# Kernel tuning notes

Hardware: AMD Instinct MI355X
Metric: run time of the kernel (lower is better)

The kernel has to match this reference:

```python
import jax, jax.numpy as jnp
import numpy as np

B, C_EDGE, C_FUSED, C_SEM = 4, 64, 128, 128
H = W = 64
MASK_SIZE = 11
EPS = 1e-6


def _window_mask(h, w, mask_size):
    # M_dw: 0 inside the clipped (mask_size x mask_size) window around each query pixel, -10000 outside.
    half = mask_size // 2
    idx = jnp.arange(h * w)
    qx, qy = idx // w, idx % w
    inside = (jnp.abs(qx[:, None] - qx[None, :]) <= half) & (jnp.abs(qy[:, None] - qy[None, :]) <= half)
    return jnp.where(inside, 0.0, -10000.0).astype(jnp.float32)


def _conv1x1(x, w, b):
    # x: [b, cin, h, w], w: [cout, cin]
    return jnp.einsum('bchw,oc->bohw', x, w) + b[None, :, None, None]


def _proj1d(x, w, b):
    # x: [b, cin, n], w: [cout, cin]
    return jnp.einsum('bcn,oc->bon', x, w) + b[None, :, None]


def _bilinear(x, h, w):
    # matches F.interpolate(mode='bilinear', align_corners=False)
    b, c = x.shape[0], x.shape[1]
    return jax.image.resize(x, (b, c, h, w), method='linear', antialias=False)


def setup_inputs() -> dict:
    key = jax.random.key(0)
    ks = jax.random.split(key, 13)
    s = 0.05
    return {
        'edge_features': jax.random.normal(ks[0], (B, C_EDGE, 32, 32), jnp.float32),
        'semantic_features': jax.random.normal(ks[1], (B, C_SEM, H, W), jnp.float32),
        'fused_features': jax.random.normal(ks[2], (B, C_FUSED, 32, 32), jnp.float32),
        'w_align': jax.random.normal(ks[3], (C_SEM, C_EDGE), jnp.float32) * s,
        'b_align': jax.random.normal(ks[4], (C_SEM,), jnp.float32) * s,
        'w_fused_align': jax.random.normal(ks[5], (C_SEM, C_FUSED), jnp.float32) * s,
        'b_fused_align': jax.random.normal(ks[6], (C_SEM,), jnp.float32) * s,
        'w_q': jax.random.normal(ks[7], (2 * C_SEM, 2 * C_SEM), jnp.float32) * s,
        'b_q': jax.random.normal(ks[8], (2 * C_SEM,), jnp.float32) * s,
        'w_k': jax.random.normal(ks[9], (2 * C_SEM, 2 * C_SEM), jnp.float32) * s,
        'b_k': jax.random.normal(ks[10], (2 * C_SEM,), jnp.float32) * s,
        'w_fusion': jax.random.normal(ks[11], (C_SEM, 2 * C_SEM), jnp.float32) * s,
        'b_fusion': jax.random.normal(ks[12], (C_SEM,), jnp.float32) * s,
    }


def reference(edge_features, semantic_features, fused_features,
              w_align, b_align, w_fused_align, b_fused_align,
              w_q, b_q, w_k, b_k, w_fusion, b_fusion):
    b, c, h, w = semantic_features.shape
    n = h * w

    edge = _conv1x1(_bilinear(edge_features, h, w), w_align, b_align)            # [b,c,h,w]
    fused = _conv1x1(_bilinear(fused_features, h, w), w_fused_align, b_fused_align)

    l2_edge = jnp.sqrt(jnp.sum(edge * edge, axis=1, keepdims=True))              # [b,1,h,w]
    l2_sem = jnp.sqrt(jnp.sum(semantic_features * semantic_features, axis=1, keepdims=True))
    similarity = jnp.sum((edge / (l2_edge + EPS)) * (semantic_features / (l2_sem + EPS)),
                         axis=1, keepdims=True)
    similarity = (similarity + 1.0) * 0.5

    density_flat = l2_edge.reshape(b, n)
    density = (jax.nn.softmax(density_flat, axis=1) * n).reshape(b, 1, h, w)

    edge_t = (edge * similarity).reshape(b, c, n)
    sem_t = (semantic_features * density).reshape(b, c, n)
    fused_t = fused.reshape(b, c, n)
    sem_raw = semantic_features.reshape(b, c, n)

    edge_cat = jnp.concatenate([edge_t, edge_t], axis=1)    # [b,2c,n]
    sem_cat = jnp.concatenate([sem_t, fused_t], axis=1)
    sem_val = jnp.concatenate([sem_raw, fused_t], axis=1)

    q = _proj1d(edge_cat, w_q, b_q)                          # [b,2c,n]
    k = _proj1d(sem_cat, w_k, b_k)

    scale = 1.0 / jnp.sqrt(jnp.float32(2 * c))
    attn = jnp.einsum('bcn,bcm->bnm', q, k) * scale          # [b,n,n]
    attn = attn + _window_mask(h, w, MASK_SIZE)
    attn = jax.nn.softmax(attn, axis=-1)

    out = jnp.einsum('bnm,bcm->bnc', attn, sem_val)          # [b,n,2c]
    out = out.reshape(b, h, w, 2 * c).transpose(0, 3, 1, 2)  # [b,2c,h,w]
    return _conv1x1(out, w_fusion, b_fusion)
```

## Files before the change

kernel.cpp:

```cpp
#include <hip/hip_runtime.h>
#include <hip/hip_bf16.h>

#define NB 4
#define C 128
#define N 4096
#define EPS 1e-6f
#define PW 80
#define PIMG 5120

typedef float f32x4 __attribute__((ext_vector_type(4)));
typedef short bf16x8 __attribute__((ext_vector_type(8)));
typedef unsigned short ushort_t;
typedef unsigned int uint_t;

__device__ __forceinline__ ushort_t f2bf(float f) {
  __hip_bfloat16 h = __float2bfloat16(f);
  return *reinterpret_cast<ushort_t*>(&h);
}

struct alignas(8) us4 { ushort_t a, b, c, d; };

__device__ __forceinline__ void conv_body(const float* __restrict__ x,
                                          const float* __restrict__ w,
                                          const float* __restrict__ bias,
                                          float* __restrict__ out,
                                          int n, int o0, int b, int CIN) {
  const float* xb = x + (size_t)(b * CIN) * 1024 + n;
  float a0 = 0.f, a1 = 0.f, a2 = 0.f, a3 = 0.f;
  for (int c = 0; c < CIN; ++c) {
    float xv = xb[(size_t)c * 1024];
    a0 += w[(o0 + 0) * CIN + c] * xv;
    a1 += w[(o0 + 1) * CIN + c] * xv;
    a2 += w[(o0 + 2) * CIN + c] * xv;
    a3 += w[(o0 + 3) * CIN + c] * xv;
  }
  size_t ob = ((size_t)b * 128 + o0) * 1024 + n;
  out[ob]        = a0 + bias[o0];
  out[ob + 1024] = a1 + bias[o0 + 1];
  out[ob + 2048] = a2 + bias[o0 + 2];
  out[ob + 3072] = a3 + bias[o0 + 3];
}

__global__ void prep_misc(const float* __restrict__ edge_f, const float* __restrict__ w_align,
                          const float* __restrict__ b_align,
                          const float* __restrict__ fused_f, const float* __restrict__ w_fal,
                          const float* __restrict__ b_fal,
                          const float* __restrict__ wq, const float* __restrict__ wk,
                          const float* __restrict__ wf,
                          ushort_t* __restrict__ wqf, ushort_t* __restrict__ wkf,
                          ushort_t* __restrict__ wff,
                          float* __restrict__ edge32, float* __restrict__ fused32,
                          float* __restrict__ dsum) {
  int bx = blockIdx.x, t = threadIdx.x;
  if (bx < 64) {
    if (bx == 0 && t < NB) dsum[t] = 0.f;
    int c = bx * 256 + t;
    int lane = c & 63;
    int mrow = lane & 15, quad = lane >> 4;
    if (c < 4096) {
      int grp = c >> 6;
      int tile = grp >> 2, kslot = grp & 3;
      int o = tile * 16 + mrow, k0 = kslot * 32 + quad * 8;
      const float* s = wq + o * 256 + k0;
      ushort_t* d = wqf + (size_t)c * 8;
#pragma unroll
      for (int j = 0; j < 8; ++j) d[j] = f2bf(s[j] + s[128 + j]);
    } else if (c < 12288) {
      int c2 = c - 4096;
      int grp = c2 >> 6;
      int tile = grp >> 3, kslot = grp & 7;
      int o = tile * 16 + mrow, k0 = kslot * 32 + quad * 8;
      const float* s = wk + o * 256 + k0;
      ushort_t* d = wkf + (size_t)c2 * 8;
#pragma unroll
      for (int j = 0; j < 8; ++j) d[j] = f2bf(s[j]);
    } else {
      int c2 = c - 12288;
      int grp = c2 >> 6;
      int tile = grp >> 3, kslot = grp & 7;
      int o = tile * 16 + mrow, k0 = kslot * 32 + quad * 8;
      const float* s = wf + o * 256 + k0;
      ushort_t* d = wff + (size_t)c2 * 8;
#pragma unroll
      for (int j = 0; j < 8; ++j) d[j] = f2bf(s[j]);
    }
  } else if (bx < 576) {
    int j = bx - 64;
    conv_body(edge_f, w_align, b_align, edge32, (j & 3) * 256 + t, ((j >> 2) & 31) * 4, j >> 7, 64);
  } else {
    int j = bx - 576;
    conv_body(fused_f, w_fal, b_fal, fused32, (j & 3) * 256 + t, ((j >> 2) & 31) * 4, j >> 7, 128);
  }
}

__global__ __launch_bounds__(256) void prep_acts(const float* __restrict__ edge32,
                                                 const float* __restrict__ fused32,
                                                 const float* __restrict__ sem,
                                                 ushort_t* __restrict__ xt_edge,
                                                 ushort_t* __restrict__ xt_sem,
                                                 ushort_t* __restrict__ xt_fused,
                                                 float* __restrict__ simb,
                                                 float* __restrict__ l2e,
                                                 float* __restrict__ dsum) {
  int b = blockIdx.y, bx = blockIdx.x;
  int y = bx >> 1, xh = (bx & 1) * 32;
  int t = threadIdx.x;
  int nl = t & 31, cg = t >> 5;
  int x = xh + nl;
  int yy0 = (y & 1) ? (y >> 1) : (y >> 1) - 1;
  float fy = (y & 1) ? 0.25f : 0.75f;
  int y0c = max(yy0, 0), y1c = min(yy0 + 1, 31);
  int xx0 = (x & 1) ? (x >> 1) : (x >> 1) - 1;
  float fx = (x & 1) ? 0.25f : 0.75f;
  int x0c = max(xx0, 0), x1c = min(xx0 + 1, 31);

  __shared__ uint_t se[32][65], ssm[32][65], sf[32][65];
  __shared__ float red[4][3][32];

  float ee = 0.f, ssum = 0.f, es = 0.f;
#pragma unroll 2
  for (int p = 0; p < 8; ++p) {
    float evs[2], fvs[2], svs[2];
#pragma unroll
    for (int u = 0; u < 2; ++u) {
      int c = cg * 16 + p * 2 + u;
      const float* ip = edge32 + ((size_t)(b * 128 + c)) * 1024;
      float e00 = ip[y0c * 32 + x0c], e01 = ip[y0c * 32 + x1c];
      float e10 = ip[y1c * 32 + x0c], e11 = ip[y1c * 32 + x1c];
      float ev = (1.f - fy) * ((1.f - fx) * e00 + fx * e01) + fy * ((1.f - fx) * e10 + fx * e11);
      const float* fp = fused32 + ((size_t)(b * 128 + c)) * 1024;
      float f00 = fp[y0c * 32 + x0c], f01 = fp[y0c * 32 + x1c];
      float f10 = fp[y1c * 32 + x0c], f11 = fp[y1c * 32 + x1c];
      float fv = (1.f - fy) * ((1.f - fx) * f00 + fx * f01) + fy * ((1.f - fx) * f10 + fx * f11);
      float sv = sem[((size_t)(b * 128 + c)) * 4096 + y * 64 + x];
      ee += ev * ev; ssum += sv * sv; es += ev * sv;
      evs[u] = ev; fvs[u] = fv; svs[u] = sv;
    }
    int col = cg * 8 + p;
    se[nl][col]  = (uint_t)f2bf(evs[0]) | ((uint_t)f2bf(evs[1]) << 16);
    sf[nl][col]  = (uint_t)f2bf(fvs[0]) | ((uint_t)f2bf(fvs[1]) << 16);
    ssm[nl][col] = (uint_t)f2bf(svs[0]) | ((uint_t)f2bf(svs[1]) << 16);
  }
  ee += __shfl_xor(ee, 32, 64); ssum += __shfl_xor(ssum, 32, 64); es += __shfl_xor(es, 32, 64);
  int w = t >> 6, lane = t & 63;
  if (lane < 32) { red[w][0][lane] = ee; red[w][1][lane] = ssum; red[w][2][lane] = es; }
  __syncthreads();
  int base_n = b * 4096 + y * 64 + xh;
#pragma unroll
  for (int rep = 0; rep < 8; ++rep) {
    int d = rep * 256 + t;
    int r = d >> 6, cp = d & 63;
    ((uint_t*)xt_edge)[(size_t)(base_n + r) * 64 + cp] = se[r][cp];
    ((uint_t*)xt_sem)[(size_t)(base_n + r) * 64 + cp] = ssm[r][cp];
    ((uint_t*)xt_fused)[(size_t)(base_n + r) * 64 + cp] = sf[r][cp];
  }
  if (t < 32) {
    float E = 0.f, S = 0.f, X = 0.f;
#pragma unroll
    for (int w2 = 0; w2 < 4; ++w2) { E += red[w2][0][t]; S += red[w2][1][t]; X += red[w2][2][t]; }
    float le = sqrtf(E), ls = sqrtf(S);
    simb[base_n + t] = (X / ((le + EPS) * (ls + EPS)) + 1.f) * 0.5f;
    l2e[base_n + t] = le;
    float pe = expf(le - 16.f);
#pragma unroll
    for (int m2 = 16; m2; m2 >>= 1) pe += __shfl_xor(pe, m2, 64);
    if (t == 0) atomicAdd(&dsum[b], pe);
  }
}

__global__ __launch_bounds__(256) void gemm_kv(const ushort_t* __restrict__ xt_sem,
                                               const ushort_t* __restrict__ xt_fused,
                                               const ushort_t* __restrict__ wkf,
                                               const ushort_t* __restrict__ wff,
                                               const float* __restrict__ b_k,
                                               const float* __restrict__ l2e,
                                               const float* __restrict__ dsum,
                                               ushort_t* __restrict__ ktb,
                                               ushort_t* __restrict__ v2b) {
  int bx = blockIdx.x, bI = blockIdx.y;
  int t = threadIdx.x, w = t >> 6, lane = t & 63;
  int mrow = lane & 15, quad = lane >> 4;
  __shared__ __align__(16) ushort_t stg[16896];

  if (bx < 64) {
    int y = bx, n0 = y * 64, o0 = w * 64;
    float dscale = 4096.f / dsum[bI];
    for (int nt = 0; nt < 4; ++nt) {
      int n0t = n0 + nt * 16;
      const ushort_t* bS = xt_sem + ((size_t)bI * N + n0t + mrow) * 128 + quad * 8;
      const ushort_t* bF = xt_fused + ((size_t)bI * N + n0t + mrow) * 128 + quad * 8;
      f32x4 accL[4], accR[4];
#pragma unroll
      for (int i = 0; i < 4; ++i) { accL[i] = (f32x4){0.f,0.f,0.f,0.f}; accR[i] = (f32x4){0.f,0.f,0.f,0.f}; }
#pragma unroll
      for (int kk = 0; kk < 4; ++kk) {
        bf16x8 bfr = *(const bf16x8*)(bS + kk * 32);
#pragma unroll
        for (int i = 0; i < 4; ++i) {
          bf16x8 afr = *(const bf16x8*)(wkf + (size_t)((((w * 4 + i) * 8) + kk) * 64 + lane) * 8);
          accL[i] = __builtin_amdgcn_mfma_f32_16x16x32_bf16(afr, bfr, accL[i], 0, 0, 0);
        }
      }
#pragma unroll
      for (int kk = 0; kk < 4; ++kk) {
        bf16x8 bfr = *(const bf16x8*)(bF + kk * 32);
#pragma unroll
        for (int i = 0; i < 4; ++i) {
          bf16x8 afr = *(const bf16x8*)(wkf + (size_t)((((w * 4 + i) * 8) + 4 + kk) * 64 + lane) * 8);
          accR[i] = __builtin_amdgcn_mfma_f32_16x16x32_bf16(afr, bfr, accR[i], 0, 0, 0);
        }
      }
      int n = n0t + mrow;
      float dv = expf(l2e[bI * N + n] - 16.f) * dscale;
#pragma unroll
      for (int i = 0; i < 4; ++i) {
        int o = o0 + i * 16 + quad * 4;
        float4 bk = *(const float4*)(b_k + o);
        us4 pk = { f2bf(accL[i][0] * dv + accR[i][0] + bk.x),
                   f2bf(accL[i][1] * dv + accR[i][1] + bk.y),
                   f2bf(accL[i][2] * dv + accR[i][2] + bk.z),
                   f2bf(accL[i][3] * dv + accR[i][3] + bk.w) };
        *(us4*)&stg[(nt * 16 + mrow) * 264 + o] = pk;
      }
    }
    __syncthreads();
    int np0 = y * PW + 8;
#pragma unroll
    for (int r = 0; r < 8; ++r) {
      int cidx = r * 256 + t;
      int row = cidx >> 5, cc = cidx & 31;
      *(bf16x8*)(ktb + ((size_t)bI * PIMG + np0 + row) * 256 + cc * 8) =
          *(const bf16x8*)&stg[row * 264 + cc * 8];
    }
  } else {
    int y = bx - 64, n0 = y * 64, o0 = w * 32;
    for (int nt = 0; nt < 4; ++nt) {
      int n0t = n0 + nt * 16;
      const ushort_t* bS = xt_sem + ((size_t)bI * N + n0t + mrow) * 128 + quad * 8;
      const ushort_t* bF = xt_fused + ((size_t)bI * N + n0t + mrow) * 128 + quad * 8;
      f32x4 accL[2], accR[2];
#pragma unroll
      for (int i = 0; i < 2; ++i) { accL[i] = (f32x4){0.f,0.f,0.f,0.f}; accR[i] = (f32x4){0.f,0.f,0.f,0.f}; }
#pragma unroll
      for (int kk = 0; kk < 4; ++kk) {
        bf16x8 bfr = *(const bf16x8*)(bS + kk * 32);
#pragma unroll
        for (int i = 0; i < 2; ++i) {
          bf16x8 afr = *(const bf16x8*)(wff + (size_t)((((w * 2 + i) * 8) + kk) * 64 + lane) * 8);
          accL[i] = __builtin_amdgcn_mfma_f32_16x16x32_bf16(afr, bfr, accL[i], 0, 0, 0);
        }
      }
#pragma unroll
      for (int kk = 0; kk < 4; ++kk) {
        bf16x8 bfr = *(const bf16x8*)(bF + kk * 32);
#pragma unroll
        for (int i = 0; i < 2; ++i) {
          bf16x8 afr = *(const bf16x8*)(wff + (size_t)((((w * 2 + i) * 8) + 4 + kk) * 64 + lane) * 8);
          accR[i] = __builtin_amdgcn_mfma_f32_16x16x32_bf16(afr, bfr, accR[i], 0, 0, 0);
        }
      }
#pragma unroll
      for (int i = 0; i < 2; ++i) {
#pragma unroll
        for (int r = 0; r < 4; ++r) {
          int ch = o0 + i * 16 + quad * 4 + r;
          stg[ch * 72 + nt * 16 + mrow] = f2bf(accL[i][r] + accR[i][r]);
        }
      }
    }
    __syncthreads();
    int np0 = y * PW + 8;
#pragma unroll
    for (int r = 0; r < 4; ++r) {
      int cidx = r * 256 + t;
      int ch = cidx >> 3, seg = cidx & 7;
      *(bf16x8*)(v2b + ((size_t)bI * 128 + ch) * PIMG + np0 + seg * 8) =
          *(const bf16x8*)&stg[ch * 72 + seg * 8];
    }
  }
}

__global__ __launch_bounds__(256) void attn_kernel(const ushort_t* __restrict__ xt_edge,
                                                   const ushort_t* __restrict__ wqf,
                                                   const float* __restrict__ b_q,
                                                   const float* __restrict__ simb,
                                                   const ushort_t* __restrict__ ktb,
                                                   const ushort_t* __restrict__ v2b,
                                                   const float* __restrict__ b_fusion,
                                                   float* __restrict__ out) {
  int L = blockIdx.x;
  int xcd = L & 7, j = L >> 3;
  int b = xcd >> 1;
  int ty0 = (((xcd & 1) << 3) + (j >> 4)) * 4;
  int tx0 = (j & 15) * 4;
  int y0 = max(ty0 - 5, 0), y1 = min(ty0 + 8, 63);
  int nh = y1 - y0 + 1;
  int x0a = tx0 - 8 - ((tx0 & 4) ? 4 : 0);
  int cb = x0a + 8;
  int ntq = (nh * 3 + 1) >> 1;
  int npv = (nh * 3 + 3) >> 2;

  __shared__ ushort_t pst[16][352];
  __shared__ __align__(16) ushort_t qs[4096];
  __shared__ float redm[4][16], reds[4][16];

  int t = threadIdx.x, w = t >> 6, lane = t & 63;
  int l15 = lane & 15, quad = lane >> 4;

  if (ntq * 16 < npv * 32) pst[t & 15][ntq * 16 + (t >> 4)] = 0;

  int nq_l = (ty0 + (l15 >> 2)) * 64 + tx0 + (l15 & 3);

  {
    const ushort_t* bp = xt_edge + ((size_t)b * N + nq_l) * 128 + quad * 8;
    f32x4 qacc[4];
#pragma unroll
    for (int i = 0; i < 4; ++i) qacc[i] = (f32x4){0.f, 0.f, 0.f, 0.f};
#pragma unroll
    for (int kk = 0; kk < 4; ++kk) {
      bf16x8 bfr = *(const bf16x8*)(bp + kk * 32);
#pragma unroll
      for (int i = 0; i < 4; ++i) {
        bf16x8 afr = *(const bf16x8*)(wqf + (size_t)((((w * 4 + i) * 4) + kk) * 64 + lane) * 8);
        qacc[i] = __builtin_amdgcn_mfma_f32_16x16x32_bf16(afr, bfr, qacc[i], 0, 0, 0);
      }
    }
    float sv = simb[b * N + nq_l];
#pragma unroll
    for (int i = 0; i < 4; ++i) {
      int o = w * 64 + i * 16 + quad * 4;
      float4 bq = *(const float4*)(b_q + o);
      us4 pk = { f2bf(sv * qacc[i][0] + bq.x), f2bf(sv * qacc[i][1] + bq.y),
                 f2bf(sv * qacc[i][2] + bq.z), f2bf(sv * qacc[i][3] + bq.w) };
      int kk2 = o >> 5, q2 = (o >> 3) & 3;
      int lane2 = l15 + 16 * q2;
      *(us4*)&qs[((kk2 * 64 + lane2) * 8) + (o & 7)] = pk;
    }
  }
  __syncthreads();

  bf16x8 qfr[8];
#pragma unroll
  for (int ks = 0; ks < 8; ++ks) qfr[ks] = *(const bf16x8*)&qs[(ks * 64 + lane) * 8];

  int qy = ty0 + (l15 >> 2), qx = tx0 + (l15 & 3);

  const ushort_t* kb = ktb + (size_t)b * PIMG * 256;
  f32x4 sc[6];
#pragma unroll
  for (int i = 0; i < 6; ++i) {
    int tq = w + i * 4;
    if (tq >= ntq) break;
    int key = tq * 16 + l15;
    int ry = (key * 2731) >> 16;
    int rx = key - ry * 24;
    int yy = min(y0 + ry, 63);
    const ushort_t* krow = kb + (size_t)(yy * PW + cb + rx) * 256 + quad * 8;
    f32x4 acc = (f32x4){0.f, 0.f, 0.f, 0.f};
#pragma unroll
    for (int ks = 0; ks < 8; ++ks) {
      bf16x8 afr = *(const bf16x8*)(krow + ks * 32);
      acc = __builtin_amdgcn_mfma_f32_16x16x32_bf16(afr, qfr[ks], acc, 0, 0, 0);
    }
    sc[i] = acc;
  }
  float mymax = -1e30f;
#pragma unroll
  for (int i = 0; i < 6; ++i) {
    int tq = w + i * 4;
    if (tq >= ntq) break;
#pragma unroll
    for (int r = 0; r < 4; ++r) {
      int key = tq * 16 + quad * 4 + r;
      int ry = (key * 2731) >> 16;
      int rx = key - ry * 24;
      int x = x0a + rx;
      int dy = y0 + ry - qy, dx = x - qx;
      float s = -1e30f;
      if (ry < nh && dy >= -5 && dy <= 5 && dx >= -5 && dx <= 5 && x >= 0 && x <= 63)
        s = sc[i][r] * 0.0625f;
      sc[i][r] = s;
      mymax = fmaxf(mymax, s);
    }
  }
  mymax = fmaxf(mymax, __shfl_xor(mymax, 16, 64));
  mymax = fmaxf(mymax, __shfl_xor(mymax, 32, 64));
  if (quad == 0) redm[w][l15] = mymax;
  __syncthreads();
  float gmax = fmaxf(fmaxf(redm[0][l15], redm[1][l15]), fmaxf(redm[2][l15], redm[3][l15]));
  float mysum = 0.f;
#pragma unroll
  for (int i = 0; i < 6; ++i) {
    int tq = w + i * 4;
    if (tq >= ntq) break;
#pragma unroll
    for (int r = 0; r < 4; ++r) {
      float e = expf(sc[i][r] - gmax);
      sc[i][r] = e;
      mysum += e;
    }
  }
  mysum += __shfl_xor(mysum, 16, 64);
  mysum += __shfl_xor(mysum, 32, 64);
  if (quad == 0) reds[w][l15] = mysum;
#pragma unroll
  for (int i = 0; i < 6; ++i) {
    int tq = w + i * 4;
    if (tq >= ntq) break;
    uint_t p01 = (uint_t)f2bf(sc[i][0]) | ((uint_t)f2bf(sc[i][1]) << 16);
    uint_t p23 = (uint_t)f2bf(sc[i][2]) | ((uint_t)f2bf(sc[i][3]) << 16);
    *(uint_t*)(&pst[l15][tq * 16 + quad * 4]) = p01;
    *(uint_t*)(&pst[l15][tq * 16 + quad * 4 + 2]) = p23;
  }
  __syncthreads();

  float rinv = 1.f / (reds[0][l15] + reds[1][l15] + reds[2][l15] + reds[3][l15]);

  const ushort_t* vb = v2b + (size_t)b * 128 * PIMG;
#pragma unroll
  for (int half = 0; half < 2; ++half) {
    int ch0 = half * 64 + w * 16;
    const ushort_t* vrow = vb + (size_t)(ch0 + l15) * PIMG;
    f32x4 acc = (f32x4){0.f, 0.f, 0.f, 0.f};
    for (int ks = 0; ks < npv; ++ks) {
      int kst = ks * 32 + quad * 8;
      int ry = (kst * 2731) >> 16;
      int rxs = kst - ry * 24;
      int yy = min(y0 + ry, 63);
      bf16x8 av = *(const bf16x8*)(vrow + yy * PW + cb + rxs);
      bf16x8 bp2 = *(const bf16x8*)(&pst[l15][kst]);
      acc = __builtin_amdgcn_mfma_f32_16x16x32_bf16(av, bp2, acc, 0, 0, 0);
    }
    int chg = ch0 + quad * 4;
#pragma unroll
    for (int r = 0; r < 4; ++r)
      out[((size_t)b * 128 + chg + r) * N + nq_l] = acc[r] * rinv + b_fusion[chg + r];
  }
}

extern "C" void kernel_launch(void* const* d_in, const int* in_sizes, int n_in,
                              void* d_out, int out_size, void* d_ws, size_t ws_size,
                              hipStream_t stream) {
  (void)in_sizes; (void)n_in; (void)out_size; (void)ws_size;
  const float* edge_f  = (const float*)d_in[0];
  const float* sem     = (const float*)d_in[1];
  const float* fused_f = (const float*)d_in[2];
  const float* w_align = (const float*)d_in[3];
  const float* b_align = (const float*)d_in[4];
  const float* w_fal   = (const float*)d_in[5];
  const float* b_fal   = (const float*)d_in[6];
  const float* w_q     = (const float*)d_in[7];
  const float* b_q     = (const float*)d_in[8];
  const float* w_k     = (const float*)d_in[9];
  const float* b_k     = (const float*)d_in[10];
  const float* w_fus   = (const float*)d_in[11];
  const float* b_fus   = (const float*)d_in[12];
  float* out = (float*)d_out;

  float* ws = (float*)d_ws;
  float* edge32   = ws;
  float* fused32  = ws + 524288;
  float* simb     = ws + 1048576;
  float* l2e      = ws + 1064960;
  float* dsum     = ws + 1081344;
  ushort_t* xt_edge  = (ushort_t*)(ws + 1097728);
  ushort_t* xt_sem   = (ushort_t*)(ws + 2146304);
  ushort_t* xt_fused = (ushort_t*)(ws + 3194880);
  ushort_t* wqf      = (ushort_t*)(ws + 4243456);
  ushort_t* wkf      = (ushort_t*)(ws + 4259840);
  ushort_t* wff      = (ushort_t*)(ws + 4292608);
  ushort_t* ktb      = (ushort_t*)(ws + 4308992);
  ushort_t* v2b      = (ushort_t*)(ws + 6930432);

  prep_misc<<<1088, 256, 0, stream>>>(edge_f, w_align, b_align, fused_f, w_fal, b_fal,
                                      w_q, w_k, w_fus, wqf, wkf, wff, edge32, fused32, dsum);
  prep_acts<<<dim3(128, NB), 256, 0, stream>>>(edge32, fused32, sem,
                                               xt_edge, xt_sem, xt_fused, simb, l2e, dsum);
  gemm_kv<<<dim3(128, NB), 256, 0, stream>>>(xt_sem, xt_fused, wkf, wff, b_k,
                                             l2e, dsum, ktb, v2b);
  attn_kernel<<<1024, 256, 0, stream>>>(xt_edge, wqf, b_q, simb, ktb, v2b, b_fus, out);
}
```

Baseline: 167.3 us.

## Fuse Q and V projections into prep, double query tile per attention block

Moves the Q projection (scaled by similarity) and the V projection out of the attention and gemm kernels into prep_acts, computed straight from the shared-memory staged activations. This removes the xt_edge round trip and the recomputation of Q in every attention block. The K-only gemm now launches half as many blocks. Attention blocks now cover 32 queries (two 16-row slabs sharing each K/V fragment load) instead of 16, halving the grid and reusing K/V reads. The cost is a larger qtb buffer in global memory, more register pressure from two accumulator sets, and a heavier prep kernel.

```diff
diff --git a/kernel.cpp b/kernel.cpp
--- a/kernel.cpp
+++ b/kernel.cpp
@@ -96,12 +96,16 @@
 __global__ __launch_bounds__(256) void prep_acts(const float* __restrict__ edge32,
                                                  const float* __restrict__ fused32,
                                                  const float* __restrict__ sem,
-                                                 ushort_t* __restrict__ xt_edge,
+                                                 const ushort_t* __restrict__ wqf,
+                                                 const ushort_t* __restrict__ wff,
+                                                 const float* __restrict__ b_q,
                                                  ushort_t* __restrict__ xt_sem,
                                                  ushort_t* __restrict__ xt_fused,
                                                  float* __restrict__ simb,
                                                  float* __restrict__ l2e,
-                                                 float* __restrict__ dsum) {
+                                                 float* __restrict__ dsum,
+                                                 ushort_t* __restrict__ qtb,
+                                                 ushort_t* __restrict__ v2b) {
   int b = blockIdx.y, bx = blockIdx.x;
   int y = bx >> 1, xh = (bx & 1) * 32;
   int t = threadIdx.x;
@@ -114,8 +118,10 @@
   float fx = (x & 1) ? 0.25f : 0.75f;
   int x0c = max(xx0, 0), x1c = min(xx0 + 1, 31);
 
-  __shared__ uint_t se[32][65], ssm[32][65], sf[32][65];
+  __shared__ uint_t se[32][68], ssm[32][68], sf[32][68];
   __shared__ float red[4][3][32];
+  __shared__ float simL[32];
+  __shared__ ushort_t vstg[128 * 40];
 
   float ee = 0.f, ssum = 0.f, es = 0.f;
 #pragma unroll 2
@@ -143,14 +149,15 @@
   }
   ee += __shfl_xor(ee, 32, 64); ssum += __shfl_xor(ssum, 32, 64); es += __shfl_xor(es, 32, 64);
   int w = t >> 6, lane = t & 63;
+  int l15 = lane & 15, quad = lane >> 4;
   if (lane < 32) { red[w][0][lane] = ee; red[w][1][lane] = ssum; red[w][2][lane] = es; }
   __syncthreads();
+
   int base_n = b * 4096 + y * 64 + xh;
 #pragma unroll
   for (int rep = 0; rep < 8; ++rep) {
     int d = rep * 256 + t;
     int r = d >> 6, cp = d & 63;
-    ((uint_t*)xt_edge)[(size_t)(base_n + r) * 64 + cp] = se[r][cp];
     ((uint_t*)xt_sem)[(size_t)(base_n + r) * 64 + cp] = ssm[r][cp];
     ((uint_t*)xt_fused)[(size_t)(base_n + r) * 64 + cp] = sf[r][cp];
   }
@@ -159,131 +166,152 @@
 #pragma unroll
     for (int w2 = 0; w2 < 4; ++w2) { E += red[w2][0][t]; S += red[w2][1][t]; X += red[w2][2][t]; }
     float le = sqrtf(E), ls = sqrtf(S);
-    simb[base_n + t] = (X / ((le + EPS) * (ls + EPS)) + 1.f) * 0.5f;
+    float sv = (X / ((le + EPS) * (ls + EPS)) + 1.f) * 0.5f;
+    simb[base_n + t] = sv;
+    simL[t] = sv;
     l2e[base_n + t] = le;
     float pe = expf(le - 16.f);
 #pragma unroll
     for (int m2 = 16; m2; m2 >>= 1) pe += __shfl_xor(pe, m2, 64);
     if (t == 0) atomicAdd(&dsum[b], pe);
   }
-}
-
-__global__ __launch_bounds__(256) void gemm_kv(const ushort_t* __restrict__ xt_sem,
-                                               const ushort_t* __restrict__ xt_fused,
-                                               const ushort_t* __restrict__ wkf,
-                                               const ushort_t* __restrict__ wff,
-                                               const float* __restrict__ b_k,
-                                               const float* __restrict__ l2e,
-                                               const float* __restrict__ dsum,
-                                               ushort_t* __restrict__ ktb,
-                                               ushort_t* __restrict__ v2b) {
-  int bx = blockIdx.x, bI = blockIdx.y;
+  __syncthreads();
+
+#pragma unroll
+  for (int h = 0; h < 2; ++h) {
+    f32x4 vacc[2];
+    vacc[0] = (f32x4){0.f,0.f,0.f,0.f};
+    vacc[1] = (f32x4){0.f,0.f,0.f,0.f};
+#pragma unroll
+    for (int kk = 0; kk < 4; ++kk) {
+      bf16x8 bfr = *(const bf16x8*)&ssm[h * 16 + l15][kk * 16 + quad * 4];
+#pragma unroll
+      for (int i = 0; i < 2; ++i) {
+        bf16x8 afr = *(const bf16x8*)(wff + (size_t)(((w + i * 4) * 8 + kk) * 64 + lane) * 8);
+        vacc[i] = __builtin_amdgcn_mfma_f32_16x16x32_bf16(afr, bfr, vacc[i], 0, 0, 0);
+      }
+    }
+#pragma unroll
+    for (int kk = 0; kk < 4; ++kk) {
+      bf16x8 bfr = *(const bf16x8*)&sf[h * 16 + l15][kk * 16 + quad * 4];
+#pragma unroll
+      for (int i = 0; i < 2; ++i) {
+        bf16x8 afr = *(const bf16x8*)(wff + (size_t)(((w + i * 4) * 8 + 4 + kk) * 64 + lane) * 8);
+        vacc[i] = __builtin_amdgcn_mfma_f32_16x16x32_bf16(afr, bfr, vacc[i], 0, 0, 0);
+      }
+    }
+#pragma unroll
+    for (int i = 0; i < 2; ++i) {
+#pragma unroll
+      for (int r = 0; r < 4; ++r) {
+        int ch = (w + i * 4) * 16 + quad * 4 + r;
+        vstg[ch * 40 + h * 16 + l15] = f2bf(vacc[i][r]);
+      }
+    }
+  }
+
+#pragma unroll
+  for (int h = 0; h < 2; ++h) {
+    f32x4 qacc[4];
+#pragma unroll
+    for (int i = 0; i < 4; ++i) qacc[i] = (f32x4){0.f,0.f,0.f,0.f};
+#pragma unroll
+    for (int kk = 0; kk < 4; ++kk) {
+      bf16x8 bfr = *(const bf16x8*)&se[h * 16 + l15][kk * 16 + quad * 4];
+#pragma unroll
+      for (int i = 0; i < 4; ++i) {
+        bf16x8 afr = *(const bf16x8*)(wqf + (size_t)(((w * 4 + i) * 4 + kk) * 64 + lane) * 8);
+        qacc[i] = __builtin_amdgcn_mfma_f32_16x16x32_bf16(afr, bfr, qacc[i], 0, 0, 0);
+      }
+    }
+    int px = h * 16 + l15;
+    float sv = simL[px];
+    int n = y * 64 + xh + px;
+#pragma unroll
+    for (int i = 0; i < 4; ++i) {
+      int o = (w * 4 + i) * 16 + quad * 4;
+      float4 bq = *(const float4*)(b_q + o);
+      us4 pk = { f2bf(sv * qacc[i][0] + bq.x), f2bf(sv * qacc[i][1] + bq.y),
+                 f2bf(sv * qacc[i][2] + bq.z), f2bf(sv * qacc[i][3] + bq.w) };
+      *(us4*)(qtb + ((size_t)b * N + n) * 256 + o) = pk;
+    }
+  }
+
+  __syncthreads();
+  int np0 = y * PW + 8 + xh;
+#pragma unroll
+  for (int r2 = 0; r2 < 2; ++r2) {
+    int idx = r2 * 256 + t;
+    int ch = idx >> 2, seg = idx & 3;
+    *(bf16x8*)(v2b + ((size_t)b * 128 + ch) * PIMG + np0 + seg * 8) =
+        *(const bf16x8*)&vstg[ch * 40 + seg * 8];
+  }
+}
+
+__global__ __launch_bounds__(256) void gemm_k(const ushort_t* __restrict__ xt_sem,
+                                              const ushort_t* __restrict__ xt_fused,
+                                              const ushort_t* __restrict__ wkf,
+                                              const float* __restrict__ b_k,
+                                              const float* __restrict__ l2e,
+                                              const float* __restrict__ dsum,
+                                              ushort_t* __restrict__ ktb) {
+  int y = blockIdx.x, bI = blockIdx.y;
   int t = threadIdx.x, w = t >> 6, lane = t & 63;
   int mrow = lane & 15, quad = lane >> 4;
   __shared__ __align__(16) ushort_t stg[16896];
 
-  if (bx < 64) {
-    int y = bx, n0 = y * 64, o0 = w * 64;
-    float dscale = 4096.f / dsum[bI];
-    for (int nt = 0; nt < 4; ++nt) {
-      int n0t = n0 + nt * 16;
-      const ushort_t* bS = xt_sem + ((size_t)bI * N + n0t + mrow) * 128 + quad * 8;
-      const ushort_t* bF = xt_fused + ((size_t)bI * N + n0t + mrow) * 128 + quad * 8;
-      f32x4 accL[4], accR[4];
-#pragma unroll
-      for (int i = 0; i < 4; ++i) { accL[i] = (f32x4){0.f,0.f,0.f,0.f}; accR[i] = (f32x4){0.f,0.f,0.f,0.f}; }
-#pragma unroll
-      for (int kk = 0; kk < 4; ++kk) {
-        bf16x8 bfr = *(const bf16x8*)(bS + kk * 32);
-#pragma unroll
-        for (int i = 0; i < 4; ++i) {
-          bf16x8 afr = *(const bf16x8*)(wkf + (size_t)((((w * 4 + i) * 8) + kk) * 64 + lane) * 8);
-          accL[i] = __builtin_amdgcn_mfma_f32_16x16x32_bf16(afr, bfr, accL[i], 0, 0, 0);
-        }
+  int n0 = y * 64, o0 = w * 64;
+  float dscale = 4096.f / dsum[bI];
+  for (int nt = 0; nt < 4; ++nt) {
+    int n0t = n0 + nt * 16;
+    const ushort_t* bS = xt_sem + ((size_t)bI * N + n0t + mrow) * 128 + quad * 8;
+    const ushort_t* bF = xt_fused + ((size_t)bI * N + n0t + mrow) * 128 + quad * 8;
+    f32x4 accL[4], accR[4];
+#pragma unroll
+    for (int i = 0; i < 4; ++i) { accL[i] = (f32x4){0.f,0.f,0.f,0.f}; accR[i] = (f32x4){0.f,0.f,0.f,0.f}; }
+#pragma unroll
+    for (int kk = 0; kk < 4; ++kk) {
+      bf16x8 bfr = *(const bf16x8*)(bS + kk * 32);
+#pragma unroll
+      for (int i = 0; i < 4; ++i) {
+        bf16x8 afr = *(const bf16x8*)(wkf + (size_t)((((w * 4 + i) * 8) + kk) * 64 + lane) * 8);
+        accL[i] = __builtin_amdgcn_mfma_f32_16x16x32_bf16(afr, bfr, accL[i], 0, 0, 0);
       }
-#pragma unroll
-      for (int kk = 0; kk < 4; ++kk) {
-        bf16x8 bfr = *(const bf16x8*)(bF + kk * 32);
-#pragma unroll
-        for (int i = 0; i < 4; ++i) {
-          bf16x8 afr = *(const bf16x8*)(wkf + (size_t)((((w * 4 + i) * 8) + 4 + kk) * 64 + lane) * 8);
-          accR[i] = __builtin_amdgcn_mfma_f32_16x16x32_bf16(afr, bfr, accR[i], 0, 0, 0);
-        }
+    }
+#pragma unroll
+    for (int kk = 0; kk < 4; ++kk) {
+      bf16x8 bfr = *(const bf16x8*)(bF + kk * 32);
+#pragma unroll
+      for (int i = 0; i < 4; ++i) {
+        bf16x8 afr = *(const bf16x8*)(wkf + (size_t)((((w * 4 + i) * 8) + 4 + kk) * 64 + lane) * 8);
+        accR[i] = __builtin_amdgcn_mfma_f32_16x16x32_bf16(afr, bfr, accR[i], 0, 0, 0);
       }
-      int n = n0t + mrow;
-      float dv = expf(l2e[bI * N + n] - 16.f) * dscale;
-#pragma unroll
-      for (int i = 0; i < 4; ++i) {
-        int o = o0 + i * 16 + quad * 4;
-        float4 bk = *(const float4*)(b_k + o);
-        us4 pk = { f2bf(accL[i][0] * dv + accR[i][0] + bk.x),
-                   f2bf(accL[i][1] * dv + accR[i][1] + bk.y),
-                   f2bf(accL[i][2] * dv + accR[i][2] + bk.z),
-                   f2bf(accL[i][3] * dv + accR[i][3] + bk.w) };
-        *(us4*)&stg[(nt * 16 + mrow) * 264 + o] = pk;
-      }
-    }
-    __syncthreads();
-    int np0 = y * PW + 8;
-#pragma unroll
-    for (int r = 0; r < 8; ++r) {
-      int cidx = r * 256 + t;
-      int row = cidx >> 5, cc = cidx & 31;
-      *(bf16x8*)(ktb + ((size_t)bI * PIMG + np0 + row) * 256 + cc * 8) =
-          *(const bf16x8*)&stg[row * 264 + cc * 8];
-    }
-  } else {
-    int y = bx - 64, n0 = y * 64, o0 = w * 32;
-    for (int nt = 0; nt < 4; ++nt) {
-      int n0t = n0 + nt * 16;
-      const ushort_t* bS = xt_sem + ((size_t)bI * N + n0t + mrow) * 128 + quad * 8;
-      const ushort_t* bF = xt_fused + ((size_t)bI * N + n0t + mrow) * 128 + quad * 8;
-      f32x4 accL[2], accR[2];
-#pragma unroll
-      for (int i = 0; i < 2; ++i) { accL[i] = (f32x4){0.f,0.f,0.f,0.f}; accR[i] = (f32x4){0.f,0.f,0.f,0.f}; }
-#pragma unroll
-      for (int kk = 0; kk < 4; ++kk) {
-        bf16x8 bfr = *(const bf16x8*)(bS + kk * 32);
-#pragma unroll
-        for (int i = 0; i < 2; ++i) {
-          bf16x8 afr = *(const bf16x8*)(wff + (size_t)((((w * 2 + i) * 8) + kk) * 64 + lane) * 8);
-          accL[i] = __builtin_amdgcn_mfma_f32_16x16x32_bf16(afr, bfr, accL[i], 0, 0, 0);
-        }
-      }
-#pragma unroll
-      for (int kk = 0; kk < 4; ++kk) {
-        bf16x8 bfr = *(const bf16x8*)(bF + kk * 32);
-#pragma unroll
-        for (int i = 0; i < 2; ++i) {
-          bf16x8 afr = *(const bf16x8*)(wff + (size_t)((((w * 2 + i) * 8) + 4 + kk) * 64 + lane) * 8);
-          accR[i] = __builtin_amdgcn_mfma_f32_16x16x32_bf16(afr, bfr, accR[i], 0, 0, 0);
-        }
-      }
-#pragma unroll
-      for (int i = 0; i < 2; ++i) {
-#pragma unroll
-        for (int r = 0; r < 4; ++r) {
-          int ch = o0 + i * 16 + quad * 4 + r;
-          stg[ch * 72 + nt * 16 + mrow] = f2bf(accL[i][r] + accR[i][r]);
-        }
-      }
-    }
-    __syncthreads();
-    int np0 = y * PW + 8;
-#pragma unroll
-    for (int r = 0; r < 4; ++r) {
-      int cidx = r * 256 + t;
-      int ch = cidx >> 3, seg = cidx & 7;
-      *(bf16x8*)(v2b + ((size_t)bI * 128 + ch) * PIMG + np0 + seg * 8) =
-          *(const bf16x8*)&stg[ch * 72 + seg * 8];
-    }
-  }
-}
-
-__global__ __launch_bounds__(256) void attn_kernel(const ushort_t* __restrict__ xt_edge,
-                                                   const ushort_t* __restrict__ wqf,
-                                                   const float* __restrict__ b_q,
-                                                   const float* __restrict__ simb,
+    }
+    int n = n0t + mrow;
+    float dv = expf(l2e[bI * N + n] - 16.f) * dscale;
+#pragma unroll
+    for (int i = 0; i < 4; ++i) {
+      int o = o0 + i * 16 + quad * 4;
+      float4 bk = *(const float4*)(b_k + o);
+      us4 pk = { f2bf(accL[i][0] * dv + accR[i][0] + bk.x),
+                 f2bf(accL[i][1] * dv + accR[i][1] + bk.y),
+                 f2bf(accL[i][2] * dv + accR[i][2] + bk.z),
+                 f2bf(accL[i][3] * dv + accR[i][3] + bk.w) };
+      *(us4*)&stg[(nt * 16 + mrow) * 264 + o] = pk;
+    }
+  }
+  __syncthreads();
+  int np0 = y * PW + 8;
+#pragma unroll
+  for (int r = 0; r < 8; ++r) {
+    int cidx = r * 256 + t;
+    int row = cidx >> 5, cc = cidx & 31;
+    *(bf16x8*)(ktb + ((size_t)bI * PIMG + np0 + row) * 256 + cc * 8) =
+        *(const bf16x8*)&stg[row * 264 + cc * 8];
+  }
+}
+
+__global__ __launch_bounds__(256) void attn_kernel(const ushort_t* __restrict__ qtb,
                                                    const ushort_t* __restrict__ ktb,
                                                    const ushort_t* __restrict__ v2b,
                                                    const float* __restrict__ b_fusion,
@@ -291,62 +319,41 @@
   int L = blockIdx.x;
   int xcd = L & 7, j = L >> 3;
   int b = xcd >> 1;
-  int ty0 = (((xcd & 1) << 3) + (j >> 4)) * 4;
-  int tx0 = (j & 15) * 4;
+  int ty0 = (((xcd & 1) << 3) + (j >> 3)) * 4;
+  int tx0 = (j & 7) * 8;
   int y0 = max(ty0 - 5, 0), y1 = min(ty0 + 8, 63);
   int nh = y1 - y0 + 1;
-  int x0a = tx0 - 8 - ((tx0 & 4) ? 4 : 0);
-  int cb = x0a + 8;
+  int x0a = tx0 - 8, cb = tx0;
   int ntq = (nh * 3 + 1) >> 1;
   int npv = (nh * 3 + 3) >> 2;
 
-  __shared__ ushort_t pst[16][352];
-  __shared__ __align__(16) ushort_t qs[4096];
-  __shared__ float redm[4][16], reds[4][16];
+  __shared__ ushort_t pst[32][352];
+  __shared__ float redm[4][2][16], reds[4][2][16];
 
   int t = threadIdx.x, w = t >> 6, lane = t & 63;
   int l15 = lane & 15, quad = lane >> 4;
 
-  if (ntq * 16 < npv * 32) pst[t & 15][ntq * 16 + (t >> 4)] = 0;
-
-  int nq_l = (ty0 + (l15 >> 2)) * 64 + tx0 + (l15 & 3);
-
+  int gap = npv * 32 - ntq * 16;
+  for (int idx = t; idx < 32 * gap; idx += 256)
+    pst[idx & 31][ntq * 16 + (idx >> 5)] = 0;
+
+  int n_s0 = (ty0 + (l15 >> 3)) * 64 + tx0 + (l15 & 7);
+  int n_s1 = n_s0 + 128;
+  bf16x8 qfr[2][8];
   {
-    const ushort_t* bp = xt_edge + ((size_t)b * N + nq_l) * 128 + quad * 8;
-    f32x4 qacc[4];
-#pragma unroll
-    for (int i = 0; i < 4; ++i) qacc[i] = (f32x4){0.f, 0.f, 0.f, 0.f};
-#pragma unroll
-    for (int kk = 0; kk < 4; ++kk) {
-      bf16x8 bfr = *(const bf16x8*)(bp + kk * 32);
-#pragma unroll
-      for (int i = 0; i < 4; ++i) {
-        bf16x8 afr = *(const bf16x8*)(wqf + (size_t)((((w * 4 + i) * 4) + kk) * 64 + lane) * 8);
-        qacc[i] = __builtin_amdgcn_mfma_f32_16x16x32_bf16(afr, bfr, qacc[i], 0, 0, 0);
-      }
-    }
-    float sv = simb[b * N + nq_l];
-#pragma unroll
-    for (int i = 0; i < 4; ++i) {
-      int o = w * 64 + i * 16 + quad * 4;
-      float4 bq = *(const float4*)(b_q + o);
-      us4 pk = { f2bf(sv * qacc[i][0] + bq.x), f2bf(sv * qacc[i][1] + bq.y),
-                 f2bf(sv * qacc[i][2] + bq.z), f2bf(sv * qacc[i][3] + bq.w) };
-      int kk2 = o >> 5, q2 = (o >> 3) & 3;
-      int lane2 = l15 + 16 * q2;
-      *(us4*)&qs[((kk2 * 64 + lane2) * 8) + (o & 7)] = pk;
-    }
-  }
-  __syncthreads();
-
-  bf16x8 qfr[8];
-#pragma unroll
-  for (int ks = 0; ks < 8; ++ks) qfr[ks] = *(const bf16x8*)&qs[(ks * 64 + lane) * 8];
-
-  int qy = ty0 + (l15 >> 2), qx = tx0 + (l15 & 3);
+    const ushort_t* q0 = qtb + ((size_t)b * N + n_s0) * 256 + quad * 8;
+    const ushort_t* q1 = qtb + ((size_t)b * N + n_s1) * 256 + quad * 8;
+#pragma unroll
+    for (int ks = 0; ks < 8; ++ks) {
+      qfr[0][ks] = *(const bf16x8*)(q0 + ks * 32);
+      qfr[1][ks] = *(const bf16x8*)(q1 + ks * 32);
+    }
+  }
+  int qx = tx0 + (l15 & 7);
+  int qy0 = ty0 + (l15 >> 3);
 
   const ushort_t* kb = ktb + (size_t)b * PIMG * 256;
-  f32x4 sc[6];
+  f32x4 sc[6][2];
 #pragma unroll
   for (int i = 0; i < 6; ++i) {
     int tq = w + i * 4;
@@ -356,15 +363,16 @@
     int rx = key - ry * 24;
     int yy = min(y0 + ry, 63);
     const ushort_t* krow = kb + (size_t)(yy * PW + cb + rx) * 256 + quad * 8;
-    f32x4 acc = (f32x4){0.f, 0.f, 0.f, 0.f};
+    f32x4 a0 = (f32x4){0.f,0.f,0.f,0.f}, a1 = (f32x4){0.f,0.f,0.f,0.f};
 #pragma unroll
     for (int ks = 0; ks < 8; ++ks) {
       bf16x8 afr = *(const bf16x8*)(krow + ks * 32);
-      acc = __builtin_amdgcn_mfma_f32_16x16x32_bf16(afr, qfr[ks], acc, 0, 0, 0);
-    }
-    sc[i] = acc;
-  }
-  float mymax = -1e30f;
+      a0 = __builtin_amdgcn_mfma_f32_16x16x32_bf16(afr, qfr[0][ks], a0, 0, 0, 0);
+      a1 = __builtin_amdgcn_mfma_f32_16x16x32_bf16(afr, qfr[1][ks], a1, 0, 0, 0);
+    }
+    sc[i][0] = a0; sc[i][1] = a1;
+  }
+  float mymax0 = -1e30f, mymax1 = -1e30f;
 #pragma unroll
   for (int i = 0; i < 6; ++i) {
     int tq = w + i * 4;
@@ -375,66 +383,83 @@
       int ry = (key * 2731) >> 16;
       int rx = key - ry * 24;
       int x = x0a + rx;
-      int dy = y0 + ry - qy, dx = x - qx;
-      float s = -1e30f;
-      if (ry < nh && dy >= -5 && dy <= 5 && dx >= -5 && dx <= 5 && x >= 0 && x <= 63)
-        s = sc[i][r] * 0.0625f;
-      sc[i][r] = s;
-      mymax = fmaxf(mymax, s);
-    }
-  }
-  mymax = fmaxf(mymax, __shfl_xor(mymax, 16, 64));
-  mymax = fmaxf(mymax, __shfl_xor(mymax, 32, 64));
-  if (quad == 0) redm[w][l15] = mymax;
+      int dx = x - qx;
+      bool xok = (dx >= -5) && (dx <= 5) && (x >= 0) && (x <= 63) && (ry < nh);
+      int dy0 = y0 + ry - qy0;
+      float s0 = (xok && dy0 >= -5 && dy0 <= 5) ? sc[i][0][r] * 0.0625f : -1e30f;
+      int dy1 = dy0 - 2;
+      float s1 = (xok && dy1 >= -5 && dy1 <= 5) ? sc[i][1][r] * 0.0625f : -1e30f;
+      sc[i][0][r] = s0; sc[i][1][r] = s1;
+      mymax0 = fmaxf(mymax0, s0); mymax1 = fmaxf(mymax1, s1);
+    }
+  }
+  mymax0 = fmaxf(mymax0, __shfl_xor(mymax0, 16, 64));
+  mymax0 = fmaxf(mymax0, __shfl_xor(mymax0, 32, 64));
+  mymax1 = fmaxf(mymax1, __shfl_xor(mymax1, 16, 64));
+  mymax1 = fmaxf(mymax1, __shfl_xor(mymax1, 32, 64));
+  if (quad == 0) { redm[w][0][l15] = mymax0; redm[w][1][l15] = mymax1; }
   __syncthreads();
-  float gmax = fmaxf(fmaxf(redm[0][l15], redm[1][l15]), fmaxf(redm[2][l15], redm[3][l15]));
-  float mysum = 0.f;
+  float gmax0 = fmaxf(fmaxf(redm[0][0][l15], redm[1][0][l15]), fmaxf(redm[2][0][l15], redm[3][0][l15]));
+  float gmax1 = fmaxf(fmaxf(redm[0][1][l15], redm[1][1][l15]), fmaxf(redm[2][1][l15], redm[3][1][l15]));
+  float mysum0 = 0.f, mysum1 = 0.f;
 #pragma unroll
   for (int i = 0; i < 6; ++i) {
     int tq = w + i * 4;
     if (tq >= ntq) break;
 #pragma unroll
     for (int r = 0; r < 4; ++r) {
-      float e = expf(sc[i][r] - gmax);
-      sc[i][r] = e;
-      mysum += e;
-    }
-  }
-  mysum += __shfl_xor(mysum, 16, 64);
-  mysum += __shfl_xor(mysum, 32, 64);
-  if (quad == 0) reds[w][l15] = mysum;
+      float e0 = expf(sc[i][0][r] - gmax0);
+      float e1 = expf(sc[i][1][r] - gmax1);
+      sc[i][0][r] = e0; sc[i][1][r] = e1;
+      mysum0 += e0; mysum1 += e1;
+    }
+  }
+  mysum0 += __shfl_xor(mysum0, 16, 64); mysum0 += __shfl_xor(mysum0, 32, 64);
+  mysum1 += __shfl_xor(mysum1, 16, 64); mysum1 += __shfl_xor(mysum1, 32, 64);
+  if (quad == 0) { reds[w][0][l15] = mysum0; reds[w][1][l15] = mysum1; }
 #pragma unroll
   for (int i = 0; i < 6; ++i) {
     int tq = w + i * 4;
     if (tq >= ntq) break;
-    uint_t p01 = (uint_t)f2bf(sc[i][0]) | ((uint_t)f2bf(sc[i][1]) << 16);
-    uint_t p23 = (uint_t)f2bf(sc[i][2]) | ((uint_t)f2bf(sc[i][3]) << 16);
-    *(uint_t*)(&pst[l15][tq * 16 + quad * 4]) = p01;
-    *(uint_t*)(&pst[l15][tq * 16 + quad * 4 + 2]) = p23;
+    int kc = tq * 16 + quad * 4;
+#pragma unroll
+    for (int s = 0; s < 2; ++s) {
+      uint_t p01 = (uint_t)f2bf(sc[i][s][0]) | ((uint_t)f2bf(sc[i][s][1]) << 16);
+      uint_t p23 = (uint_t)f2bf(sc[i][s][2]) | ((uint_t)f2bf(sc[i][s][3]) << 16);
+      *(uint_t*)(&pst[s * 16 + l15][kc]) = p01;
+      *(uint_t*)(&pst[s * 16 + l15][kc + 2]) = p23;
+    }
   }
   __syncthreads();
 
-  float rinv = 1.f / (reds[0][l15] + reds[1][l15] + reds[2][l15] + reds[3][l15]);
+  float rinv0 = 1.f / (reds[0][0][l15] + reds[1][0][l15] + reds[2][0][l15] + reds[3][0][l15]);
+  float rinv1 = 1.f / (reds[0][1][l15] + reds[1][1][l15] + reds[2][1][l15] + reds[3][1][l15]);
 
   const ushort_t* vb = v2b + (size_t)b * 128 * PIMG;
 #pragma unroll
   for (int half = 0; half < 2; ++half) {
     int ch0 = half * 64 + w * 16;
     const ushort_t* vrow = vb + (size_t)(ch0 + l15) * PIMG;
-    f32x4 acc = (f32x4){0.f, 0.f, 0.f, 0.f};
+    f32x4 acc0 = (f32x4){0.f,0.f,0.f,0.f}, acc1 = (f32x4){0.f,0.f,0.f,0.f};
     for (int ks = 0; ks < npv; ++ks) {
       int kst = ks * 32 + quad * 8;
       int ry = (kst * 2731) >> 16;
       int rxs = kst - ry * 24;
       int yy = min(y0 + ry, 63);
       bf16x8 av = *(const bf16x8*)(vrow + yy * PW + cb + rxs);
-      bf16x8 bp2 = *(const bf16x8*)(&pst[l15][kst]);
-      acc = __builtin_amdgcn_mfma_f32_16x16x32_bf16(av, bp2, acc, 0, 0, 0);
+      bf16x8 bp0 = *(const bf16x8*)(&pst[l15][kst]);
+      bf16x8 bp1 = *(const bf16x8*)(&pst[16 + l15][kst]);
+      acc0 = __builtin_amdgcn_mfma_f32_16x16x32_bf16(av, bp0, acc0, 0, 0, 0);
+      acc1 = __builtin_amdgcn_mfma_f32_16x16x32_bf16(av, bp1, acc1, 0, 0, 0);
     }
     int chg = ch0 + quad * 4;
-#pragma unroll
-    for (int r = 0; r < 4; ++r)
-      out[((size_t)b * 128 + chg + r) * N + nq_l] = acc[r] * rinv + b_fusion[chg + r];
+    float4 bf4 = *(const float4*)(b_fusion + chg);
+    float bfa[4] = {bf4.x, bf4.y, bf4.z, bf4.w};
+#pragma unroll
+    for (int r = 0; r < 4; ++r) {
+      out[((size_t)b * 128 + chg + r) * N + n_s0] = acc0[r] * rinv0 + bfa[r];
+      out[((size_t)b * 128 + chg + r) * N + n_s1] = acc1[r] * rinv1 + bfa[r];
+    }
   }
 }
 
@@ -463,20 +488,19 @@
   float* simb     = ws + 1048576;
   float* l2e      = ws + 1064960;
   float* dsum     = ws + 1081344;
-  ushort_t* xt_edge  = (ushort_t*)(ws + 1097728);
-  ushort_t* xt_sem   = (ushort_t*)(ws + 2146304);
-  ushort_t* xt_fused = (ushort_t*)(ws + 3194880);
-  ushort_t* wqf      = (ushort_t*)(ws + 4243456);
-  ushort_t* wkf      = (ushort_t*)(ws + 4259840);
-  ushort_t* wff      = (ushort_t*)(ws + 4292608);
-  ushort_t* ktb      = (ushort_t*)(ws + 4308992);
-  ushort_t* v2b      = (ushort_t*)(ws + 6930432);
+  ushort_t* xt_sem   = (ushort_t*)(ws + 1097728);
+  ushort_t* xt_fused = (ushort_t*)(ws + 2146304);
+  ushort_t* wqf      = (ushort_t*)(ws + 3194880);
+  ushort_t* wkf      = (ushort_t*)(ws + 3211264);
+  ushort_t* wff      = (ushort_t*)(ws + 3244032);
+  ushort_t* qtb      = (ushort_t*)(ws + 3260416);
+  ushort_t* ktb      = (ushort_t*)(ws + 5357568);
+  ushort_t* v2b      = (ushort_t*)(ws + 7979008);
 
   prep_misc<<<1088, 256, 0, stream>>>(edge_f, w_align, b_align, fused_f, w_fal, b_fal,
                                       w_q, w_k, w_fus, wqf, wkf, wff, edge32, fused32, dsum);
-  prep_acts<<<dim3(128, NB), 256, 0, stream>>>(edge32, fused32, sem,
-                                               xt_edge, xt_sem, xt_fused, simb, l2e, dsum);
-  gemm_kv<<<dim3(128, NB), 256, 0, stream>>>(xt_sem, xt_fused, wkf, wff, b_k,
-                                             l2e, dsum, ktb, v2b);
-  attn_kernel<<<1024, 256, 0, stream>>>(xt_edge, wqf, b_q, simb, ktb, v2b, b_fus, out);
-}
+  prep_acts<<<dim3(128, NB), 256, 0, stream>>>(edge32, fused32, sem, wqf, wff, b_q,
+                                               xt_sem, xt_fused, simb, l2e, dsum, qtb, v2b);
+  gemm_k<<<dim3(64, NB), 256, 0, stream>>>(xt_sem, xt_fused, wkf, b_k, l2e, dsum, ktb);
+  attn_kernel<<<512, 256, 0, stream>>>(qtb, ktb, v2b, b_fus, out);
+}
```

Result: faster. 161.1 us (-3.7%).
